# Optimization experiments

Measured on AMD Instinct MI355X. Metric: run time of the kernel, lower is better.

The kernel has to match this reference:

```python
import jax, jax.numpy as jnp
import numpy as np

DIM = 2048
N_HEADS = 32
HEAD_DIM = DIM // N_HEADS  # 64
ROT_DIM = 32               # partial_rotary_factor = 32/head_dim
ROPE_THETA = 1000000.0
T = 2048
QKV_DIM = 3 * DIM


def setup_inputs() -> dict:
    key = jax.random.key(0)
    ks = jax.random.split(key, 8)
    inp = {
        "positions": jnp.arange(T, dtype=jnp.int32),
        "hidden_states": jax.random.normal(ks[0], (T, DIM), dtype=jnp.float32),
        "Wqkv": jax.random.normal(ks[1], (QKV_DIM, DIM), dtype=jnp.float32) * 0.02,
        "bqkv": jax.random.normal(ks[2], (QKV_DIM,), dtype=jnp.float32) * 0.02,
        "Wout": jax.random.normal(ks[3], (DIM, DIM), dtype=jnp.float32) * 0.02,
        "bout": jax.random.normal(ks[4], (DIM,), dtype=jnp.float32) * 0.02,
        "tau_alpha": jax.random.normal(ks[5], (N_HEADS,), dtype=jnp.float32) * 0.1,
        "tau_wq": jax.random.normal(ks[6], (N_HEADS, QKV_DIM), dtype=jnp.float32) * 0.02,
        "tau_wv": jax.random.normal(ks[7], (N_HEADS, QKV_DIM), dtype=jnp.float32) * 0.02,
    }
    return inp


def _rope_neox(x, positions):
    # x: [T, H, D]; rotate first ROT_DIM dims, neox (half-split) style
    half = ROT_DIM // 2
    inv_freq = 1.0 / (ROPE_THETA ** (jnp.arange(0, ROT_DIM, 2, dtype=jnp.float32) / ROT_DIM))
    ang = positions.astype(jnp.float32)[:, None] * inv_freq[None, :]  # [T, half]
    cos = jnp.cos(ang)[:, None, :]  # [T, 1, half]
    sin = jnp.sin(ang)[:, None, :]
    x1 = x[..., :half]
    x2 = x[..., half:ROT_DIM]
    rot = jnp.concatenate([x1 * cos - x2 * sin, x2 * cos + x1 * sin], axis=-1)
    return jnp.concatenate([rot, x[..., ROT_DIM:]], axis=-1)


def reference(positions, hidden_states, Wqkv, bqkv, Wout, bout, tau_alpha, tau_wq, tau_wv):
    T_, H, D = hidden_states.shape[0], N_HEADS, HEAD_DIM
    qkv = hidden_states @ Wqkv.T + bqkv  # [T, 3*DIM]
    q, k, v = jnp.split(qkv, [DIM, 2 * DIM], axis=-1)

    # tau gating (exact-erf gelu, matching torch F.gelu default)
    tok_feat = jax.nn.gelu(qkv, approximate=False)
    tok_q = jnp.tanh(tok_feat @ tau_wq.T)  # [T, H]
    tok_v = jnp.tanh(tok_feat @ tau_wv.T)
    pos_log = jnp.log(jnp.clip(positions.astype(jnp.float32) + 1.0, 1e-6))  # [T]
    tau_pos = 1.0 + (jax.nn.sigmoid(tau_alpha[None, :] * pos_log[:, None]) - 0.5)  # [T, H]
    tau_q = tok_q + tau_pos
    tau_v = tok_v + tau_pos

    q = q.reshape(T_, H, D) * tau_q[:, :, None]
    k = k.reshape(T_, H, D)
    v = v.reshape(T_, H, D) * tau_v[:, :, None]

    q = _rope_neox(q, positions)
    k = _rope_neox(k, positions)

    # causal attention
    scale = D ** -0.5
    scores = jnp.einsum("thd,shd->hts", q, k) * scale  # [H, T, T]
    causal = positions[:, None] >= positions[None, :]   # [T, T]
    scores = jnp.where(causal[None, :, :], scores, jnp.finfo(scores.dtype).min)
    probs = jax.nn.softmax(scores, axis=-1)
    attn = jnp.einsum("hts,shd->thd", probs, v).reshape(T_, DIM)

    return attn @ Wout.T + bout
```

## Files before the change

kernel.cpp:

```cpp
#include <hip/hip_runtime.h>
#include <math.h>


typedef __bf16 bf16x8 __attribute__((ext_vector_type(8)));
typedef float floatx4 __attribute__((ext_vector_type(4)));
typedef unsigned short ushort8v __attribute__((ext_vector_type(8)));

__device__ __forceinline__ unsigned short f2b(float x) {
    unsigned int b = __float_as_uint(x);
    b = b + 0x7FFFu + ((b >> 16) & 1u);
    return (unsigned short)(b >> 16);
}
__device__ __forceinline__ unsigned short f2b_trunc(float x) {
    return (unsigned short)(__float_as_uint(x) >> 16);
}
__device__ __forceinline__ float b2f(unsigned short u) {
    return __uint_as_float(((unsigned int)u) << 16);
}
__device__ __forceinline__ float gelu_f(float x) {
    return 0.5f * x * (1.0f + erff(x * 0.70710678118654752440f));
}
__device__ __forceinline__ float fexp2(float x) {
    return __builtin_amdgcn_exp2f(x);
}
__device__ __forceinline__ floatx4 mfma16(bf16x8 a, bf16x8 b, floatx4 c) {
    return __builtin_amdgcn_mfma_f32_16x16x32_bf16(a, b, c, 0, 0, 0);
}
__device__ __forceinline__ void gl2lds16(const unsigned short* g, unsigned short* l) {
    __builtin_amdgcn_global_load_lds(
        (__attribute__((address_space(1))) void*)g,
        (__attribute__((address_space(3))) void*)l, 16, 0, 0);
}

__constant__ float INV_FREQ[16] = {
    1.0f, 0.42169650342858224f, 0.17782794100389228f, 0.074989420933245582f,
    0.031622776601683791f, 0.013335214321633240f, 0.0056234132519034908f,
    0.0023713737056616552f, 0.001f, 4.2169650342858224e-4f,
    1.7782794100389228e-4f, 7.4989420933245582e-5f, 3.1622776601683791e-5f,
    1.3335214321633240e-5f, 5.6234132519034908e-6f, 2.3713737056616552e-6f
};

__constant__ unsigned char CHUNK_QT[40] = {
    15,15,15, 14,14,14, 13,13,13, 12,12,12, 11,11, 10,10, 9,9, 8,8, 7,6,5,4,
    15,11,7,3, 14,10,6,2, 13,9,5,1, 12,8,4,0};
__constant__ unsigned char CHUNK_C[40] = {
    0,1,2, 0,1,2, 0,1,2, 0,1,2, 0,1, 0,1, 0,1, 0,1, 0,0,0,0,
    3,2,1,0, 3,2,1,0, 3,2,1,0, 3,2,1,0};

__global__ __launch_bounds__(256) void cvt3_f32_bf16(
    const float* __restrict__ s0, unsigned short* __restrict__ d0, int n0,
    const float* __restrict__ s1, unsigned short* __restrict__ d1, int n1,
    const float* __restrict__ s2, unsigned short* __restrict__ d2, int n2) {
    int i = blockIdx.x * 256 + threadIdx.x;
    const float* s; unsigned short* d;
    if (i < n0)           { s = s0; d = d0; }
    else if (i < n0 + n1) { i -= n0; s = s1; d = d1; }
    else                  { i -= n0 + n1; s = s2; d = d2; if (i >= n2) return; }
    const float4* sp = reinterpret_cast<const float4*>(s) + (size_t)i * 2;
    float4 a = sp[0], b = sp[1];
    ushort8v r;
    r[0] = f2b(a.x); r[1] = f2b(a.y); r[2] = f2b(a.z); r[3] = f2b(a.w);
    r[4] = f2b(b.x); r[5] = f2b(b.y); r[6] = f2b(b.z); r[7] = f2b(b.w);
    *(reinterpret_cast<ushort8v*>(d) + i) = r;
}

__global__ __launch_bounds__(512, 2) void gemm_qkv_8ph(
    const unsigned short* __restrict__ A, const unsigned short* __restrict__ B,
    const float* __restrict__ bias, unsigned short* __restrict__ P,
    int M, int N, int K) {
    __shared__ unsigned short Ls[2][4][8192];
    const int tid = threadIdx.x;
    const int wave = tid >> 6, lane = tid & 63;
    const int row16 = lane & 15, quad = lane >> 4;
    const int wrow = wave >> 2, wcol = wave & 3;
    const int bm0 = blockIdx.y * 256, bn0 = blockIdx.x * 256;
    const int NT = K >> 6;

    floatx4 acc[8][4] = {};

    auto stage_half = [&](int kt, int hf) {
        const unsigned short* mat = (hf & 1) ? B : A;
        const int rbase = (hf & 1) ? bn0 : bm0;
        const int colb = kt * 64 + (hf >> 1) * 32;
        unsigned short* dst = &Ls[kt & 1][hf][0];
        #pragma unroll
        for (int rd = 0; rd < 2; ++rd) {
            int g = tid + rd * 512;
            int rl = g & 7, c4 = (g >> 3) & 3, r8 = g >> 5;
            gl2lds16(mat + (size_t)(rbase + r8 * 8 + rl) * K + colb + c4 * 8,
                     dst + g * 8);
        }
    };

    #pragma unroll
    for (int h = 0; h < 7; ++h) stage_half(h >> 2, h & 3);
    asm volatile("s_waitcnt vmcnt(6)" ::: "memory");
    __builtin_amdgcn_s_barrier();

    const int ra = wrow * 128 + row16;
    const int rb = wcol * 64 + row16;
    const int aoff = (ra >> 3) * 256 + quad * 64 + (ra & 7) * 8;
    const int boff = (rb >> 3) * 256 + quad * 64 + (rb & 7) * 8;

    bf16x8 Aping[4], Apong[4], Bping[4], Bpong[4];
    #pragma unroll
    for (int i = 0; i < 4; ++i) {
        Aping[i] = *reinterpret_cast<const bf16x8*>(&Ls[0][0][aoff + i * 512]);
        Bping[i] = *reinterpret_cast<const bf16x8*>(&Ls[0][1][boff + i * 512]);
    }

    for (int kt = 0; kt < NT; ++kt) {
        const int bsel = kt & 1;
        asm volatile("s_waitcnt lgkmcnt(0)" ::: "memory");
        __builtin_amdgcn_sched_barrier(0);
        #pragma unroll
        for (int i = 0; i < 4; ++i)
            Apong[i] = *reinterpret_cast<const bf16x8*>(&Ls[bsel][0][aoff + (4 + i) * 512]);
        __builtin_amdgcn_sched_barrier(0);
        __builtin_amdgcn_s_setprio(1);
        #pragma unroll
        for (int mt = 0; mt < 4; ++mt)
            #pragma unroll
            for (int nt = 0; nt < 4; ++nt)
                acc[mt][nt] = mfma16(Aping[mt], Bping[nt], acc[mt][nt]);
        __builtin_amdgcn_s_setprio(0);
        __builtin_amdgcn_s_barrier();
        if (kt + 1 < NT) stage_half(kt + 1, 3);
        asm volatile("s_waitcnt lgkmcnt(0)" ::: "memory");
        __builtin_amdgcn_sched_barrier(0);
        #pragma unroll
        for (int i = 0; i < 4; ++i) {
            Aping[i] = *reinterpret_cast<const bf16x8*>(&Ls[bsel][2][aoff + i * 512]);
            Bpong[i] = *reinterpret_cast<const bf16x8*>(&Ls[bsel][3][boff + i * 512]);
        }
        __builtin_amdgcn_sched_barrier(0);
        __builtin_amdgcn_s_setprio(1);
        #pragma unroll
        for (int mt = 0; mt < 4; ++mt)
            #pragma unroll
            for (int nt = 0; nt < 4; ++nt)
                acc[4 + mt][nt] = mfma16(Apong[mt], Bping[nt], acc[4 + mt][nt]);
        __builtin_amdgcn_s_setprio(0);
        __builtin_amdgcn_s_barrier();
        if (kt + 2 < NT) stage_half(kt + 2, 0);
        asm volatile("s_waitcnt lgkmcnt(0)" ::: "memory");
        __builtin_amdgcn_sched_barrier(0);
        #pragma unroll
        for (int i = 0; i < 4; ++i)
            Apong[i] = *reinterpret_cast<const bf16x8*>(&Ls[bsel][2][aoff + (4 + i) * 512]);
        __builtin_amdgcn_sched_barrier(0);
        __builtin_amdgcn_s_setprio(1);
        #pragma unroll
        for (int mt = 0; mt < 4; ++mt)
            #pragma unroll
            for (int nt = 0; nt < 4; ++nt)
                acc[mt][nt] = mfma16(Aping[mt], Bpong[nt], acc[mt][nt]);
        __builtin_amdgcn_s_setprio(0);
        __builtin_amdgcn_s_barrier();
        if (kt + 2 < NT) stage_half(kt + 2, 1);
        if (kt <= NT - 2) {
            if (kt == NT - 2) asm volatile("s_waitcnt vmcnt(0)" ::: "memory");
            else              asm volatile("s_waitcnt vmcnt(4)" ::: "memory");
            __builtin_amdgcn_s_barrier();
        }
        asm volatile("s_waitcnt lgkmcnt(0)" ::: "memory");
        __builtin_amdgcn_sched_barrier(0);
        if (kt + 1 < NT) {
            #pragma unroll
            for (int i = 0; i < 4; ++i) {
                Aping[i] = *reinterpret_cast<const bf16x8*>(&Ls[bsel ^ 1][0][aoff + i * 512]);
                Bping[i] = *reinterpret_cast<const bf16x8*>(&Ls[bsel ^ 1][1][boff + i * 512]);
            }
        }
        __builtin_amdgcn_sched_barrier(0);
        __builtin_amdgcn_s_setprio(1);
        #pragma unroll
        for (int mt = 0; mt < 4; ++mt)
            #pragma unroll
            for (int nt = 0; nt < 4; ++nt)
                acc[4 + mt][nt] = mfma16(Apong[mt], Bpong[nt], acc[4 + mt][nt]);
        __builtin_amdgcn_s_setprio(0);
        __builtin_amdgcn_s_barrier();
        if (kt + 2 < NT) stage_half(kt + 2, 2);
    }

    #pragma unroll
    for (int mt = 0; mt < 8; ++mt) {
        #pragma unroll
        for (int nt = 0; nt < 4; ++nt) {
            int gc = bn0 + wcol * 64 + nt * 16 + row16;
            float bv = bias[gc];
            int gr0 = bm0 + wrow * 128 + mt * 16 + quad * 4;
            #pragma unroll
            for (int i = 0; i < 4; ++i)
                P[(size_t)(gr0 + i) * N + gc] = f2b(acc[mt][nt][i] + bv);
        }
    }
}

template <int BM, int BN, bool OUT_BF16>
__global__ __launch_bounds__(256) void gemm_bf16_bt(
    const unsigned short* __restrict__ A, const unsigned short* __restrict__ B,
    const float* __restrict__ bias, void* __restrict__ Cout,
    int M, int N, int K) {
    constexpr int MT = BM / 32, NT = BN / 32;
    __shared__ unsigned short As[BM * 64];
    __shared__ unsigned short Bs[BN * 64];
    const int tid = threadIdx.x;
    const int wave = tid >> 6, lane = tid & 63;
    const int row16 = lane & 15, quad = lane >> 4;
    const int wm = (wave >> 1) * (BM / 2), wn = (wave & 1) * (BN / 2);
    const int bm0 = blockIdx.y * BM, bn0 = blockIdx.x * BN;
    const int rl = lane & 7, cl = lane >> 3;

    floatx4 acc[MT][NT] = {};

    for (int k0 = 0; k0 < K; k0 += 64) {
        __syncthreads();
        #pragma unroll
        for (int j = 0; j < BM / 32; ++j) {
            int unit = wave * (BM / 32) + j;
            const unsigned short* ga = A + (size_t)(bm0 + unit * 8 + rl) * K + k0 + cl * 8;
            gl2lds16(ga, &As[unit * 512 + lane * 8]);
        }
        #pragma unroll
        for (int j = 0; j < BN / 32; ++j) {
            int unit = wave * (BN / 32) + j;
            const unsigned short* gb = B + (size_t)(bn0 + unit * 8 + rl) * K + k0 + cl * 8;
            gl2lds16(gb, &Bs[unit * 512 + lane * 8]);
        }
        __syncthreads();

        #pragma unroll
        for (int ks = 0; ks < 2; ++ks) {
            bf16x8 af[MT], bfr[NT];
            #pragma unroll
            for (int mt = 0; mt < MT; ++mt) {
                int r = wm + mt * 16 + row16;
                af[mt] = *reinterpret_cast<const bf16x8*>(
                    &As[(r >> 3) * 512 + (ks * 4 + quad) * 64 + (r & 7) * 8]);
            }
            #pragma unroll
            for (int nt = 0; nt < NT; ++nt) {
                int r = wn + nt * 16 + row16;
                bfr[nt] = *reinterpret_cast<const bf16x8*>(
                    &Bs[(r >> 3) * 512 + (ks * 4 + quad) * 64 + (r & 7) * 8]);
            }
            #pragma unroll
            for (int mt = 0; mt < MT; ++mt)
                #pragma unroll
                for (int nt = 0; nt < NT; ++nt)
                    acc[mt][nt] = mfma16(af[mt], bfr[nt], acc[mt][nt]);
        }
    }

    #pragma unroll
    for (int mt = 0; mt < MT; ++mt) {
        #pragma unroll
        for (int nt = 0; nt < NT; ++nt) {
            int gc = bn0 + wn + nt * 16 + row16;
            float bv = bias[gc];
            int gr0 = bm0 + wm + mt * 16 + quad * 4;
            #pragma unroll
            for (int i = 0; i < 4; ++i) {
                float v = acc[mt][nt][i] + bv;
                if (OUT_BF16)
                    ((unsigned short*)Cout)[(size_t)(gr0 + i) * N + gc] = f2b(v);
                else
                    ((float*)Cout)[(size_t)(gr0 + i) * N + gc] = v;
            }
        }
    }
}

template <int KSPLIT>
__global__ __launch_bounds__(256) void tok_gemm_splitk(
    const unsigned short* __restrict__ A0,
    const float* __restrict__ Bq, const float* __restrict__ Bv,
    float* __restrict__ C, int K) {
    constexpr int LDT = 72;
    __shared__ unsigned short As[64 * LDT];
    __shared__ unsigned short Bs[64 * LDT];
    const int tid = threadIdx.x;
    const int wave = tid >> 6, lane = tid & 63;
    const int row16 = lane & 15, quad = lane >> 4;
    const int wm = (wave >> 1) * 32, wn = (wave & 1) * 32;
    const int bm0 = blockIdx.y * 64;
    const int kbeg = blockIdx.x * KSPLIT;

    floatx4 acc[2][2] = {};

    for (int k0 = kbeg; k0 < kbeg + KSPLIT; k0 += 64) {
        #pragma unroll
        for (int it = 0; it < 2; ++it) {
            int i = tid + it * 256;
            int r = i >> 3, c8 = i & 7;
            size_t off = (size_t)(bm0 + r) * K + k0 + c8 * 8;
            ushort8v a0 = *reinterpret_cast<const ushort8v*>(A0 + off);
            ushort8v g;
            #pragma unroll
            for (int j = 0; j < 8; ++j) g[j] = f2b(gelu_f(b2f(a0[j])));
            *reinterpret_cast<ushort8v*>(&As[r * LDT + c8 * 8]) = g;

            const float* brow = (r < 32) ? (Bq + (size_t)r * K) : (Bv + (size_t)(r - 32) * K);
            float4 w0 = *reinterpret_cast<const float4*>(brow + k0 + c8 * 8);
            float4 w1 = *reinterpret_cast<const float4*>(brow + k0 + c8 * 8 + 4);
            ushort8v wb;
            wb[0] = f2b(w0.x); wb[1] = f2b(w0.y); wb[2] = f2b(w0.z); wb[3] = f2b(w0.w);
            wb[4] = f2b(w1.x); wb[5] = f2b(w1.y); wb[6] = f2b(w1.z); wb[7] = f2b(w1.w);
            *reinterpret_cast<ushort8v*>(&Bs[r * LDT + c8 * 8]) = wb;
        }
        __syncthreads();

        #pragma unroll
        for (int ks = 0; ks < 2; ++ks) {
            bf16x8 af[2], bfr[2];
            #pragma unroll
            for (int mt = 0; mt < 2; ++mt)
                af[mt] = *reinterpret_cast<const bf16x8*>(
                    &As[(wm + mt * 16 + row16) * LDT + ks * 32 + quad * 8]);
            #pragma unroll
            for (int nt = 0; nt < 2; ++nt)
                bfr[nt] = *reinterpret_cast<const bf16x8*>(
                    &Bs[(wn + nt * 16 + row16) * LDT + ks * 32 + quad * 8]);
            #pragma unroll
            for (int mt = 0; mt < 2; ++mt)
                #pragma unroll
                for (int nt = 0; nt < 2; ++nt)
                    acc[mt][nt] = mfma16(af[mt], bfr[nt], acc[mt][nt]);
        }
        __syncthreads();
    }

    #pragma unroll
    for (int mt = 0; mt < 2; ++mt)
        #pragma unroll
        for (int nt = 0; nt < 2; ++nt) {
            int gc = wn + nt * 16 + row16;
            int gr0 = bm0 + wm + mt * 16 + quad * 4;
            #pragma unroll
            for (int i = 0; i < 4; ++i)
                atomicAdd(&C[(size_t)(gr0 + i) * 64 + gc], acc[mt][nt][i]);
        }
}

__global__ __launch_bounds__(256) void qkv_process(
    const unsigned short* __restrict__ P,
    const float* __restrict__ tok_raw, const float* __restrict__ tau_alpha,
    const int* __restrict__ positions, unsigned short* __restrict__ qh,
    unsigned short* __restrict__ kh, unsigned short* __restrict__ vpk) {
    const int h = blockIdx.y;
    const int t0 = blockIdx.x * 64;
    const int tid = threadIdx.x;
    __shared__ float vtr[64][65];
    __shared__ float tauq_s[64], tauv_s[64];

    if (tid < 64) {
        int t = t0 + tid;
        float pos = (float)positions[t];
        float pl = logf(fmaxf(pos + 1.0f, 1e-6f));
        float a = tau_alpha[h];
        float tp = 0.5f + 1.0f / (1.0f + __expf(-a * pl));
        tauq_s[tid] = tanhf(tok_raw[t * 64 + h]) + tp;
        tauv_s[tid] = tanhf(tok_raw[t * 64 + 32 + h]) + tp;
    }
    __syncthreads();

    const float QSCALE = 0.18033688011112042f;
    #pragma unroll
    for (int it = 0; it < 2; ++it) {
        int idx = tid + it * 256;
        int tl = idx >> 3, c8 = idx & 7;
        int t = t0 + tl;
        size_t rb = (size_t)t * 6144 + h * 64 + c8 * 8;
        ushort8v q0v = *reinterpret_cast<const ushort8v*>(P + rb);
        ushort8v k0v = *reinterpret_cast<const ushort8v*>(P + rb + 2048);
        ushort8v v0v = *reinterpret_cast<const ushort8v*>(P + rb + 4096);
        float tq = tauq_s[tl], tv = tauv_s[tl];
        float qo[8], ko[8];
        #pragma unroll
        for (int j = 0; j < 8; ++j) {
            qo[j] = b2f(q0v[j]) * tq;
            ko[j] = b2f(k0v[j]);
        }
        if (c8 < 4) {
            size_t rp = (size_t)t * 6144 + h * 64 + (c8 ^ 2) * 8;
            ushort8v qp0 = *reinterpret_cast<const ushort8v*>(P + rp);
            ushort8v kp0 = *reinterpret_cast<const ushort8v*>(P + rp + 2048);
            float pos = (float)positions[t];
            float sgn = (c8 < 2) ? -1.0f : 1.0f;
            #pragma unroll
            for (int j = 0; j < 8; ++j) {
                int fi = (c8 * 8 + j) & 15;
                float ang = pos * INV_FREQ[fi];
                float s, c;
                sincosf(ang, &s, &c);
                float qp = b2f(qp0[j]) * tq;
                float kp = b2f(kp0[j]);
                qo[j] = qo[j] * c + sgn * qp * s;
                ko[j] = ko[j] * c + sgn * kp * s;
            }
        }
        size_t ob = ((size_t)h * 2048 + t) * 64 + c8 * 8;
        ushort8v qw, kw;
        #pragma unroll
        for (int j = 0; j < 8; ++j) {
            qw[j] = f2b(qo[j] * QSCALE);
            kw[j] = f2b(ko[j]);
        }
        *reinterpret_cast<ushort8v*>(qh + ob) = qw;
        *reinterpret_cast<ushort8v*>(kh + ob) = kw;
        #pragma unroll
        for (int j = 0; j < 8; ++j)
            vtr[c8 * 8 + j][tl] = b2f(v0v[j]) * tv;
    }
    __syncthreads();
    #pragma unroll
    for (int it = 0; it < 2; ++it) {
        int idx = tid + it * 256;
        int d = idx >> 3, tc = (idx & 7) * 8;
        int sb = (t0 + tc) >> 5;
        int quad = (tc & 31) >> 3;
        int nt = d >> 4, m = d & 15;
        ushort8v w;
        #pragma unroll
        for (int j = 0; j < 8; ++j) w[j] = f2b(vtr[d][tc + j]);
        *reinterpret_cast<ushort8v*>(
            vpk + (size_t)h * 131072 + sb * 2048 + nt * 512 + quad * 128 + m * 8) = w;
    }
}

__global__ __launch_bounds__(256) void attn_fa(
    const unsigned short* __restrict__ qh, const unsigned short* __restrict__ kh,
    const unsigned short* __restrict__ vpk, unsigned short* __restrict__ Opart,
    float* __restrict__ ml) {
    constexpr int LD = 72;
    __shared__ unsigned short pbuf[4][2][16 * LD];
    const int b = blockIdx.x;
    const int h = (b & 7) + 8 * ((b >> 3) & 3);
    const int cpos = b >> 5;
    const int qt = CHUNK_QT[cpos], ch = CHUNK_C[cpos];
    const int q0 = qt * 128;
    const int slot = (h * 16 + qt) * 4 + ch;
    const int wave = threadIdx.x >> 6, lane = threadIdx.x & 63;
    const int m = lane & 15, quad = lane >> 4;
    const int qrow0 = q0 + wave * 32;
    const int sbeg = ch * 512;
    const int send = min(sbeg + 512, qrow0 + 32);

    bf16x8 aq[2][2];
    #pragma unroll
    for (int mt = 0; mt < 2; ++mt) {
        const unsigned short* qptr = qh + ((size_t)h * 2048 + qrow0 + mt * 16 + m) * 64;
        aq[mt][0] = *reinterpret_cast<const bf16x8*>(qptr + quad * 8);
        aq[mt][1] = *reinterpret_cast<const bf16x8*>(qptr + 32 + quad * 8);
    }
    const unsigned short* kbase = kh + (size_t)h * 2048 * 64;
    const unsigned short* vbase = vpk + (size_t)h * 131072;

    floatx4 o[2][4] = {};
    float lsum[2][4] = {};

    for (int s0 = sbeg; s0 < send; s0 += 64) {
        floatx4 sc[2][4];
        #pragma unroll
        for (int sg = 0; sg < 4; ++sg) {
            const unsigned short* kr = kbase + (size_t)(s0 + sg * 16 + m) * 64;
            bf16x8 bk0 = *reinterpret_cast<const bf16x8*>(kr + quad * 8);
            bf16x8 bk1 = *reinterpret_cast<const bf16x8*>(kr + 32 + quad * 8);
            #pragma unroll
            for (int mt = 0; mt < 2; ++mt) {
                floatx4 z = {};
                z = mfma16(aq[mt][0], bk0, z);
                z = mfma16(aq[mt][1], bk1, z);
                sc[mt][sg] = z;
            }
        }
        if (s0 + 63 > qrow0) {
            #pragma unroll
            for (int mt = 0; mt < 2; ++mt)
                #pragma unroll
                for (int sg = 0; sg < 4; ++sg)
                    #pragma unroll
                    for (int i = 0; i < 4; ++i) {
                        int t = qrow0 + mt * 16 + quad * 4 + i;
                        int s = s0 + sg * 16 + m;
                        sc[mt][sg][i] = (s > t) ? -1e30f : sc[mt][sg][i];
                    }
        }
        #pragma unroll
        for (int mt = 0; mt < 2; ++mt)
            #pragma unroll
            for (int sg = 0; sg < 4; ++sg)
                #pragma unroll
                for (int i = 0; i < 4; ++i)
                    sc[mt][sg][i] = fexp2(sc[mt][sg][i]);
        #pragma unroll
        for (int mt = 0; mt < 2; ++mt)
            #pragma unroll
            for (int i = 0; i < 4; ++i)
                lsum[mt][i] += (sc[mt][0][i] + sc[mt][1][i]) + (sc[mt][2][i] + sc[mt][3][i]);

        unsigned short* pb0 = pbuf[wave][0];
        unsigned short* pb1 = pbuf[wave][1];
        #pragma unroll
        for (int sg = 0; sg < 4; ++sg)
            #pragma unroll
            for (int i = 0; i < 4; ++i) {
                pb0[(quad * 4 + i) * LD + sg * 16 + m] = f2b_trunc(sc[0][sg][i]);
                pb1[(quad * 4 + i) * LD + sg * 16 + m] = f2b_trunc(sc[1][sg][i]);
            }
        bf16x8 ap[2][2];
        #pragma unroll
        for (int mt = 0; mt < 2; ++mt) {
            ap[mt][0] = *reinterpret_cast<const bf16x8*>(&pbuf[wave][mt][m * LD + quad * 8]);
            ap[mt][1] = *reinterpret_cast<const bf16x8*>(&pbuf[wave][mt][m * LD + 32 + quad * 8]);
        }
        #pragma unroll
        for (int c = 0; c < 2; ++c) {
            const unsigned short* vrow = vbase + ((s0 >> 5) + c) * 2048;
            #pragma unroll
            for (int nt = 0; nt < 4; ++nt) {
                bf16x8 bv = *reinterpret_cast<const bf16x8*>(vrow + nt * 512 + lane * 8);
                o[0][nt] = mfma16(ap[0][c], bv, o[0][nt]);
                o[1][nt] = mfma16(ap[1][c], bv, o[1][nt]);
            }
        }
    }

    #pragma unroll
    for (int d = 1; d < 16; d <<= 1)
        #pragma unroll
        for (int mt = 0; mt < 2; ++mt)
            #pragma unroll
            for (int i = 0; i < 4; ++i)
                lsum[mt][i] += __shfl_xor(lsum[mt][i], d, 16);
    #pragma unroll
    for (int mt = 0; mt < 2; ++mt) {
        #pragma unroll
        for (int nt = 0; nt < 4; ++nt)
            #pragma unroll
            for (int i = 0; i < 4; ++i)
                Opart[((size_t)slot * 128 + wave * 32 + mt * 16 + quad * 4 + i) * 64 + nt * 16 + m]
                    = f2b(o[mt][nt][i]);
        if (m == 0) {
            #pragma unroll
            for (int i = 0; i < 4; ++i)
                ml[(size_t)slot * 128 + wave * 32 + mt * 16 + quad * 4 + i] = lsum[mt][i];
        }
    }
}

__global__ __launch_bounds__(256) void attn_merge(
    const unsigned short* __restrict__ Opart, const float* __restrict__ ml,
    unsigned short* __restrict__ attnb) {
    const int qt = blockIdx.x, h = blockIdx.y;
    const int nc = qt / 4 + 1;
    const int tid = threadIdx.x;
    const int r = tid >> 1, dh = (tid & 1) * 32;
    const int bs = (h * 16 + qt) * 4;

    float denom = 0.0f;
    #pragma unroll
    for (int c = 0; c < 4; ++c)
        if (c < nc) denom += ml[(size_t)(bs + c) * 128 + r];
    float inv = 1.0f / denom;

    float acc[32] = {};
    #pragma unroll
    for (int c = 0; c < 4; ++c) {
        if (c < nc) {
            const unsigned short* op = Opart + ((size_t)(bs + c) * 128 + r) * 64 + dh;
            #pragma unroll
            for (int j = 0; j < 4; ++j) {
                ushort8v v = *reinterpret_cast<const ushort8v*>(op + j * 8);
                #pragma unroll
                for (int k = 0; k < 8; ++k)
                    acc[j * 8 + k] += b2f(v[k]);
            }
        }
    }
    unsigned short* dst = attnb + (size_t)(qt * 128 + r) * 2048 + h * 64 + dh;
    #pragma unroll
    for (int j = 0; j < 4; ++j) {
        ushort8v v;
        #pragma unroll
        for (int k = 0; k < 8; ++k) v[k] = f2b(acc[j * 8 + k] * inv);
        *reinterpret_cast<ushort8v*>(dst + j * 8) = v;
    }
}

extern "C" void kernel_launch(void* const* d_in, const int* in_sizes, int n_in,
                              void* d_out, int out_size, void* d_ws, size_t ws_size,
                              hipStream_t stream) {
    const int*   positions = (const int*)d_in[0];
    const float* hidden    = (const float*)d_in[1];
    const float* Wqkv      = (const float*)d_in[2];
    const float* bqkv      = (const float*)d_in[3];
    const float* Wout      = (const float*)d_in[4];
    const float* bout      = (const float*)d_in[5];
    const float* tau_alpha = (const float*)d_in[6];
    const float* tau_wq    = (const float*)d_in[7];
    const float* tau_wv    = (const float*)d_in[8];

    unsigned char* ws = (unsigned char*)d_ws;
    unsigned short* P       = (unsigned short*)(ws);
    unsigned short* Opart   = (unsigned short*)(ws);
    unsigned short* wqb     = (unsigned short*)(ws + 50331648);
    unsigned short* qh      = (unsigned short*)(ws + 50331648);
    unsigned short* kh      = (unsigned short*)(ws + 58720256);
    unsigned short* vpk     = (unsigned short*)(ws + 67108864);
    unsigned short* hb      = (unsigned short*)(ws + 75497472);
    float*          tok_raw = (float*)(ws + 75497472);
    unsigned short* attnb   = (unsigned short*)(ws + 75497472);
    float*          ml      = (float*)(ws + 83886080);
    unsigned short* wob     = (unsigned short*)(ws + 85983232);

    cvt3_f32_bf16<<<10240, 256, 0, stream>>>(
        hidden, hb, 524288, Wqkv, wqb, 1572864, Wout, wob, 524288);
    gemm_qkv_8ph<<<dim3(24, 8), 512, 0, stream>>>(
        hb, wqb, bqkv, P, 2048, 6144, 2048);
    hipMemsetAsync(tok_raw, 0, (size_t)2048 * 64 * 4, stream);
    tok_gemm_splitk<256><<<dim3(24, 32), 256, 0, stream>>>(
        P, tau_wq, tau_wv, tok_raw, 6144);
    qkv_process<<<dim3(32, 32), 256, 0, stream>>>(
        P, tok_raw, tau_alpha, positions, qh, kh, vpk);
    attn_fa<<<1280, 256, 0, stream>>>(qh, kh, vpk, Opart, ml);
    attn_merge<<<dim3(16, 32), 256, 0, stream>>>(Opart, ml, attnb);
    gemm_bf16_bt<64, 64, false><<<dim3(32, 32), 256, 0, stream>>>(
        attnb, wob, bout, d_out, 2048, 2048, 2048);
}
```

Before: 376.5 us.

## Retile QKV GEMM to 128x192 blocks with 256 threads for full CU coverage

Replaces the 256x256-tile, 512-thread QKV GEMM with a 128x192-tile, 256-thread version launched on a 32x16 grid. The aim is to remove the poor occupancy of the old 192-block grid, which leaves many CUs idle. LDS staging is restructured into a flat per-buffer layout with four phases per K-tile, double buffering and prefetch. The smaller tiles lower per-block data reuse and raise global/L2 traffic.

```diff
diff --git a/kernel.cpp b/kernel.cpp
--- a/kernel.cpp
+++ b/kernel.cpp
@@ -64,133 +64,128 @@
     *(reinterpret_cast<ushort8v*>(d) + i) = r;
 }
 
-__global__ __launch_bounds__(512, 2) void gemm_qkv_8ph(
+__global__ __launch_bounds__(256, 2) void gemm_qkv_p2(
     const unsigned short* __restrict__ A, const unsigned short* __restrict__ B,
     const float* __restrict__ bias, unsigned short* __restrict__ P,
     int M, int N, int K) {
-    __shared__ unsigned short Ls[2][4][8192];
+    __shared__ unsigned short Ls[2][20480];
     const int tid = threadIdx.x;
     const int wave = tid >> 6, lane = tid & 63;
     const int row16 = lane & 15, quad = lane >> 4;
-    const int wrow = wave >> 2, wcol = wave & 3;
-    const int bm0 = blockIdx.y * 256, bn0 = blockIdx.x * 256;
+    const int wrow = wave >> 1, wcol = wave & 1;
+    const int bm0 = blockIdx.y * 128, bn0 = blockIdx.x * 192;
     const int NT = K >> 6;
 
-    floatx4 acc[8][4] = {};
+    floatx4 acc[4][6] = {};
 
     auto stage_half = [&](int kt, int hf) {
-        const unsigned short* mat = (hf & 1) ? B : A;
-        const int rbase = (hf & 1) ? bn0 : bm0;
+        const bool isB = hf & 1;
+        const unsigned short* mat = isB ? B : A;
+        const int rbase = isB ? bn0 : bm0;
         const int colb = kt * 64 + (hf >> 1) * 32;
-        unsigned short* dst = &Ls[kt & 1][hf][0];
-        #pragma unroll
-        for (int rd = 0; rd < 2; ++rd) {
-            int g = tid + rd * 512;
+        const int hoff = ((hf & 1) ? 4096 : 0) + (hf >> 1) * 10240;
+        unsigned short* dst = &Ls[kt & 1][hoff];
+        const int nrd = isB ? 3 : 2;
+        #pragma unroll
+        for (int rd = 0; rd < 3; ++rd) {
+            if (rd >= nrd) break;
+            int g = tid + rd * 256;
             int rl = g & 7, c4 = (g >> 3) & 3, r8 = g >> 5;
             gl2lds16(mat + (size_t)(rbase + r8 * 8 + rl) * K + colb + c4 * 8,
                      dst + g * 8);
         }
     };
 
-    #pragma unroll
-    for (int h = 0; h < 7; ++h) stage_half(h >> 2, h & 3);
-    asm volatile("s_waitcnt vmcnt(6)" ::: "memory");
+    stage_half(0, 0); stage_half(0, 1); stage_half(0, 2); stage_half(0, 3);
+    stage_half(1, 0); stage_half(1, 1); stage_half(1, 2);
+    asm volatile("s_waitcnt vmcnt(7)" ::: "memory");
     __builtin_amdgcn_s_barrier();
 
-    const int ra = wrow * 128 + row16;
-    const int rb = wcol * 64 + row16;
+    const int ra = wrow * 64 + row16;
+    const int rb = wcol * 96 + row16;
     const int aoff = (ra >> 3) * 256 + quad * 64 + (ra & 7) * 8;
     const int boff = (rb >> 3) * 256 + quad * 64 + (rb & 7) * 8;
 
-    bf16x8 Aping[4], Apong[4], Bping[4], Bpong[4];
-    #pragma unroll
-    for (int i = 0; i < 4; ++i) {
-        Aping[i] = *reinterpret_cast<const bf16x8*>(&Ls[0][0][aoff + i * 512]);
-        Bping[i] = *reinterpret_cast<const bf16x8*>(&Ls[0][1][boff + i * 512]);
-    }
-
     for (int kt = 0; kt < NT; ++kt) {
         const int bsel = kt & 1;
+        bf16x8 af[4], bfr[3];
+        #pragma unroll
+        for (int mt = 0; mt < 4; ++mt)
+            af[mt] = *reinterpret_cast<const bf16x8*>(&Ls[bsel][aoff + mt * 512]);
+        #pragma unroll
+        for (int j = 0; j < 3; ++j)
+            bfr[j] = *reinterpret_cast<const bf16x8*>(&Ls[bsel][4096 + boff + j * 512]);
+        if (kt + 1 < NT) stage_half(kt + 1, 3);
+        __builtin_amdgcn_s_barrier();
         asm volatile("s_waitcnt lgkmcnt(0)" ::: "memory");
         __builtin_amdgcn_sched_barrier(0);
-        #pragma unroll
-        for (int i = 0; i < 4; ++i)
-            Apong[i] = *reinterpret_cast<const bf16x8*>(&Ls[bsel][0][aoff + (4 + i) * 512]);
+        __builtin_amdgcn_s_setprio(1);
+        #pragma unroll
+        for (int mt = 0; mt < 4; ++mt)
+            #pragma unroll
+            for (int j = 0; j < 3; ++j)
+                acc[mt][j] = mfma16(af[mt], bfr[j], acc[mt][j]);
+        __builtin_amdgcn_s_setprio(0);
+        __builtin_amdgcn_s_barrier();
+        #pragma unroll
+        for (int j = 0; j < 3; ++j)
+            bfr[j] = *reinterpret_cast<const bf16x8*>(&Ls[bsel][4096 + boff + (3 + j) * 512]);
+        if (kt + 2 < NT) stage_half(kt + 2, 0);
+        __builtin_amdgcn_s_barrier();
+        asm volatile("s_waitcnt lgkmcnt(0)" ::: "memory");
         __builtin_amdgcn_sched_barrier(0);
         __builtin_amdgcn_s_setprio(1);
         #pragma unroll
         for (int mt = 0; mt < 4; ++mt)
             #pragma unroll
-            for (int nt = 0; nt < 4; ++nt)
-                acc[mt][nt] = mfma16(Aping[mt], Bping[nt], acc[mt][nt]);
+            for (int j = 0; j < 3; ++j)
+                acc[mt][3 + j] = mfma16(af[mt], bfr[j], acc[mt][3 + j]);
         __builtin_amdgcn_s_setprio(0);
         __builtin_amdgcn_s_barrier();
-        if (kt + 1 < NT) stage_half(kt + 1, 3);
+        #pragma unroll
+        for (int mt = 0; mt < 4; ++mt)
+            af[mt] = *reinterpret_cast<const bf16x8*>(&Ls[bsel][10240 + aoff + mt * 512]);
+        #pragma unroll
+        for (int j = 0; j < 3; ++j)
+            bfr[j] = *reinterpret_cast<const bf16x8*>(&Ls[bsel][14336 + boff + j * 512]);
+        if (kt + 2 < NT) stage_half(kt + 2, 1);
+        __builtin_amdgcn_s_barrier();
         asm volatile("s_waitcnt lgkmcnt(0)" ::: "memory");
         __builtin_amdgcn_sched_barrier(0);
-        #pragma unroll
-        for (int i = 0; i < 4; ++i) {
-            Aping[i] = *reinterpret_cast<const bf16x8*>(&Ls[bsel][2][aoff + i * 512]);
-            Bpong[i] = *reinterpret_cast<const bf16x8*>(&Ls[bsel][3][boff + i * 512]);
-        }
+        __builtin_amdgcn_s_setprio(1);
+        #pragma unroll
+        for (int mt = 0; mt < 4; ++mt)
+            #pragma unroll
+            for (int j = 0; j < 3; ++j)
+                acc[mt][j] = mfma16(af[mt], bfr[j], acc[mt][j]);
+        __builtin_amdgcn_s_setprio(0);
+        __builtin_amdgcn_s_barrier();
+        #pragma unroll
+        for (int j = 0; j < 3; ++j)
+            bfr[j] = *reinterpret_cast<const bf16x8*>(&Ls[bsel][14336 + boff + (3 + j) * 512]);
+        if (kt + 2 < NT) stage_half(kt + 2, 2);
+        if (kt == NT - 2)     asm volatile("s_waitcnt vmcnt(0)" ::: "memory");
+        else if (kt < NT - 2) asm volatile("s_waitcnt vmcnt(7)" ::: "memory");
+        __builtin_amdgcn_s_barrier();
+        asm volatile("s_waitcnt lgkmcnt(0)" ::: "memory");
         __builtin_amdgcn_sched_barrier(0);
         __builtin_amdgcn_s_setprio(1);
         #pragma unroll
         for (int mt = 0; mt < 4; ++mt)
             #pragma unroll
-            for (int nt = 0; nt < 4; ++nt)
-                acc[4 + mt][nt] = mfma16(Apong[mt], Bping[nt], acc[4 + mt][nt]);
+            for (int j = 0; j < 3; ++j)
+                acc[mt][3 + j] = mfma16(af[mt], bfr[j], acc[mt][3 + j]);
         __builtin_amdgcn_s_setprio(0);
         __builtin_amdgcn_s_barrier();
-        if (kt + 2 < NT) stage_half(kt + 2, 0);
-        asm volatile("s_waitcnt lgkmcnt(0)" ::: "memory");
-        __builtin_amdgcn_sched_barrier(0);
-        #pragma unroll
-        for (int i = 0; i < 4; ++i)
-            Apong[i] = *reinterpret_cast<const bf16x8*>(&Ls[bsel][2][aoff + (4 + i) * 512]);
-        __builtin_amdgcn_sched_barrier(0);
-        __builtin_amdgcn_s_setprio(1);
-        #pragma unroll
-        for (int mt = 0; mt < 4; ++mt)
-            #pragma unroll
-            for (int nt = 0; nt < 4; ++nt)
-                acc[mt][nt] = mfma16(Aping[mt], Bpong[nt], acc[mt][nt]);
-        __builtin_amdgcn_s_setprio(0);
-        __builtin_amdgcn_s_barrier();
-        if (kt + 2 < NT) stage_half(kt + 2, 1);
-        if (kt <= NT - 2) {
-            if (kt == NT - 2) asm volatile("s_waitcnt vmcnt(0)" ::: "memory");
-            else              asm volatile("s_waitcnt vmcnt(4)" ::: "memory");
-            __builtin_amdgcn_s_barrier();
-        }
-        asm volatile("s_waitcnt lgkmcnt(0)" ::: "memory");
-        __builtin_amdgcn_sched_barrier(0);
-        if (kt + 1 < NT) {
-            #pragma unroll
-            for (int i = 0; i < 4; ++i) {
-                Aping[i] = *reinterpret_cast<const bf16x8*>(&Ls[bsel ^ 1][0][aoff + i * 512]);
-                Bping[i] = *reinterpret_cast<const bf16x8*>(&Ls[bsel ^ 1][1][boff + i * 512]);
-            }
-        }
-        __builtin_amdgcn_sched_barrier(0);
-        __builtin_amdgcn_s_setprio(1);
-        #pragma unroll
-        for (int mt = 0; mt < 4; ++mt)
-            #pragma unroll
-            for (int nt = 0; nt < 4; ++nt)
-                acc[4 + mt][nt] = mfma16(Apong[mt], Bpong[nt], acc[4 + mt][nt]);
-        __builtin_amdgcn_s_setprio(0);
-        __builtin_amdgcn_s_barrier();
-        if (kt + 2 < NT) stage_half(kt + 2, 2);
-    }
-
-    #pragma unroll
-    for (int mt = 0; mt < 8; ++mt) {
-        #pragma unroll
-        for (int nt = 0; nt < 4; ++nt) {
-            int gc = bn0 + wcol * 64 + nt * 16 + row16;
+    }
+
+    #pragma unroll
+    for (int mt = 0; mt < 4; ++mt) {
+        #pragma unroll
+        for (int nt = 0; nt < 6; ++nt) {
+            int gc = bn0 + wcol * 96 + nt * 16 + row16;
             float bv = bias[gc];
-            int gr0 = bm0 + wrow * 128 + mt * 16 + quad * 4;
+            int gr0 = bm0 + wrow * 64 + mt * 16 + quad * 4;
             #pragma unroll
             for (int i = 0; i < 4; ++i)
                 P[(size_t)(gr0 + i) * N + gc] = f2b(acc[mt][nt][i] + bv);
@@ -618,7 +613,7 @@
 
     cvt3_f32_bf16<<<10240, 256, 0, stream>>>(
         hidden, hb, 524288, Wqkv, wqb, 1572864, Wout, wob, 524288);
-    gemm_qkv_8ph<<<dim3(24, 8), 512, 0, stream>>>(
+    gemm_qkv_p2<<<dim3(32, 16), 256, 0, stream>>>(
         hb, wqb, bqkv, P, 2048, 6144, 2048);
     hipMemsetAsync(tok_raw, 0, (size_t)2048 * 64 * 4, stream);
     tok_gemm_splitk<256><<<dim3(24, 32), 256, 0, stream>>>(
```

Result: no change. 382.0 us (+1.4%).
